# Optimization experiments

Hardware: AMD Instinct MI355X
Metric: run time of the kernel (lower is better)

## Reference

```python
import jax, jax.numpy as jnp
import numpy as np

N_NODES = 4096
N_EDGES = 131072
IN_DIM = 40
HID = 128
OUT = 128
GAT_H = 2
GAT_C = 64
D_MODEL = 128
N_HEAD = 4
FF_DIM = 2048
N_LAYERS = 2
EPS = 1e-5
NEG_SLOPE = 0.2


def _layer_norm(x, g, b):
    mu = x.mean(-1, keepdims=True)
    var = ((x - mu) ** 2).mean(-1, keepdims=True)
    return (x - mu) / jnp.sqrt(var + EPS) * g + b


def _gat_conv(h, src, dst, W, a_src, a_dst, bias):
    # PyG GATConv, concat=True, eval mode (no dropout). Self loops already in (src, dst).
    N = h.shape[0]
    xw = (h @ W.T).reshape(N, GAT_H, GAT_C)          # [N, H, C]
    al_src = (xw * a_src).sum(-1)                     # [N, H]
    al_dst = (xw * a_dst).sum(-1)                     # [N, H]
    e = jax.nn.leaky_relu(al_src[src] + al_dst[dst], NEG_SLOPE)  # [E, H]
    # segment softmax over incoming edges of each dst node
    m = jax.ops.segment_max(e, dst, num_segments=N)
    ex = jnp.exp(e - m[dst])
    s = jax.ops.segment_sum(ex, dst, num_segments=N)
    alpha = ex / (s[dst] + 1e-16)                     # [E, H]
    out = jax.ops.segment_sum(xw[src] * alpha[..., None], dst, num_segments=N)
    return out.reshape(N, GAT_H * GAT_C) + bias


def _encoder_layer(x, p):
    # post-norm nn.TransformerEncoderLayer, relu FFN, eval mode
    (in_w, in_b, out_w, out_b, ln1_g, ln1_b,
     ff_w1, ff_b1, ff_w2, ff_b2, ln2_g, ln2_b) = p
    S, E = x.shape
    Dh = E // N_HEAD
    qkv = x @ in_w.T + in_b                           # [S, 3E]
    q, k, v = [t.reshape(S, N_HEAD, Dh) for t in jnp.split(qkv, 3, axis=-1)]
    scores = jnp.einsum('shd,thd->hst', q, k) / jnp.asarray(np.sqrt(Dh), x.dtype)
    attn = jax.nn.softmax(scores, axis=-1)            # [H, S, S]
    o = jnp.einsum('hst,thd->shd', attn, v).reshape(S, E) @ out_w.T + out_b
    x = _layer_norm(x + o, ln1_g, ln1_b)
    ff = jax.nn.relu(x @ ff_w1.T + ff_b1) @ ff_w2.T + ff_b2
    return _layer_norm(x + ff, ln2_g, ln2_b)


def _forward(floats, edge_index):
    (x, enc_w1, enc_b1, enc_w2, enc_b2,
     gat_w, gat_asrc, gat_adst, gat_b,
     l0_in_w, l0_in_b, l0_out_w, l0_out_b, l0_ln1_g, l0_ln1_b,
     l0_ff_w1, l0_ff_b1, l0_ff_w2, l0_ff_b2, l0_ln2_g, l0_ln2_b,
     l1_in_w, l1_in_b, l1_out_w, l1_out_b, l1_ln1_g, l1_ln1_b,
     l1_ff_w1, l1_ff_b1, l1_ff_w2, l1_ff_b2, l1_ln2_g, l1_ln2_b) = floats
    N = x.shape[0]
    # encoder MLP
    h = jax.nn.relu(x @ enc_w1.T + enc_b1) @ enc_w2.T + enc_b2
    # add one self loop per node (GATConv add_self_loops semantics)
    loop = jnp.arange(N, dtype=edge_index.dtype)
    src = jnp.concatenate([edge_index[0], loop])
    dst = jnp.concatenate([edge_index[1], loop])
    h = _gat_conv(h, src, dst, gat_w, gat_asrc, gat_adst, gat_b)
    layers = [
        (l0_in_w, l0_in_b, l0_out_w, l0_out_b, l0_ln1_g, l0_ln1_b,
         l0_ff_w1, l0_ff_b1, l0_ff_w2, l0_ff_b2, l0_ln2_g, l0_ln2_b),
        (l1_in_w, l1_in_b, l1_out_w, l1_out_b, l1_ln1_g, l1_ln1_b,
         l1_ff_w1, l1_ff_b1, l1_ff_w2, l1_ff_b2, l1_ln2_g, l1_ln2_b),
    ]
    for p in layers:
        h = _encoder_layer(h, p)
    return h


def setup_inputs() -> dict:
    key = jax.random.key(0)
    ks = jax.random.split(key, 40)
    s = 0.05
    inp = {}
    inp['x'] = jax.random.normal(ks[0], (N_NODES, IN_DIM), dtype=jnp.float32)
    # edges with src != dst (self loops added inside reference)
    src = jax.random.randint(ks[1], (N_EDGES,), 0, N_NODES)
    off = jax.random.randint(ks[2], (N_EDGES,), 1, N_NODES)
    dst = (src + off) % N_NODES
    inp['edge_index'] = jnp.stack([src, dst]).astype(jnp.int64)
    inp['enc_w1'] = jax.random.normal(ks[3], (HID, IN_DIM)) * s
    inp['enc_b1'] = jnp.zeros((HID,), jnp.float32)
    inp['enc_w2'] = jax.random.normal(ks[4], (OUT, HID)) * s
    inp['enc_b2'] = jnp.zeros((OUT,), jnp.float32)
    inp['gat_w'] = jax.random.normal(ks[5], (GAT_H * GAT_C, OUT)) * s
    inp['gat_asrc'] = jax.random.normal(ks[6], (GAT_H, GAT_C)) * s
    inp['gat_adst'] = jax.random.normal(ks[7], (GAT_H, GAT_C)) * s
    inp['gat_b'] = jnp.zeros((GAT_H * GAT_C,), jnp.float32)
    for i in range(N_LAYERS):
        k = jax.random.split(ks[8 + i], 8)
        inp[f'l{i}_in_w'] = jax.random.normal(k[0], (3 * D_MODEL, D_MODEL)) * s
        inp[f'l{i}_in_b'] = jnp.zeros((3 * D_MODEL,), jnp.float32)
        inp[f'l{i}_out_w'] = jax.random.normal(k[1], (D_MODEL, D_MODEL)) * s
        inp[f'l{i}_out_b'] = jnp.zeros((D_MODEL,), jnp.float32)
        inp[f'l{i}_ln1_g'] = jnp.ones((D_MODEL,), jnp.float32)
        inp[f'l{i}_ln1_b'] = jnp.zeros((D_MODEL,), jnp.float32)
        inp[f'l{i}_ff_w1'] = jax.random.normal(k[2], (FF_DIM, D_MODEL)) * s
        inp[f'l{i}_ff_b1'] = jnp.zeros((FF_DIM,), jnp.float32)
        inp[f'l{i}_ff_w2'] = jax.random.normal(k[3], (D_MODEL, FF_DIM)) * s
        inp[f'l{i}_ff_b2'] = jnp.zeros((D_MODEL,), jnp.float32)
        inp[f'l{i}_ln2_g'] = jnp.ones((D_MODEL,), jnp.float32)
        inp[f'l{i}_ln2_b'] = jnp.zeros((D_MODEL,), jnp.float32)
    return inp


def reference(x, edge_index, enc_w1, enc_b1, enc_w2, enc_b2,
              gat_w, gat_asrc, gat_adst, gat_b,
              l0_in_w, l0_in_b, l0_out_w, l0_out_b, l0_ln1_g, l0_ln1_b,
              l0_ff_w1, l0_ff_b1, l0_ff_w2, l0_ff_b2, l0_ln2_g, l0_ln2_b,
              l1_in_w, l1_in_b, l1_out_w, l1_out_b, l1_ln1_g, l1_ln1_b,
              l1_ff_w1, l1_ff_b1, l1_ff_w2, l1_ff_b2, l1_ln2_g, l1_ln2_b):
    floats = (x, enc_w1, enc_b1, enc_w2, enc_b2,
              gat_w, gat_asrc, gat_adst, gat_b,
              l0_in_w, l0_in_b, l0_out_w, l0_out_b, l0_ln1_g, l0_ln1_b,
              l0_ff_w1, l0_ff_b1, l0_ff_w2, l0_ff_b2, l0_ln2_g, l0_ln2_b,
              l1_in_w, l1_in_b, l1_out_w, l1_out_b, l1_ln1_g, l1_ln1_b,
              l1_ff_w1, l1_ff_b1, l1_ff_w2, l1_ff_b2, l1_ln2_g, l1_ln2_b)
    return _forward(floats, edge_index)
```

## Files before the change

### kernel.cpp

```cpp
#include <hip/hip_runtime.h>
#include <hip/hip_bf16.h>

typedef __hip_bfloat16 bf16;

#define N_NODES 4096
#define IN_DIM  40
#define DM      128
#define FF_DIM  2048
#define GAT_H   2
#define GAT_C   64
#define NHEAD   4
#define DH      32
#define LN_EPS  1e-5f
#define KSPLIT  8
#define FSPLIT  4

typedef short s8v __attribute__((ext_vector_type(8)));
typedef float f4v __attribute__((ext_vector_type(4)));

__device__ __forceinline__ float anyload(const void* p, size_t i, int isbf) {
    if (isbf) return __bfloat162float(((const bf16*)p)[i]);
    return ((const float*)p)[i];
}
__device__ __forceinline__ int geti(const int* ei, int i, int is64) {
    return is64 ? ei[2 * (size_t)i] : ei[i];
}
__device__ __forceinline__ ushort tob(float v) {
    bf16 b = __float2bfloat16(v);
    return *(ushort*)&b;
}

__global__ void probe_kernel(const void* ones_vec, const int* ei, int* flags,
                             int* __restrict__ deg) {
    int i = blockIdx.x * 256 + threadIdx.x;
    if (i < N_NODES) deg[i] = 0;
    if (i == 0) {
        unsigned u = ((const unsigned*)ones_vec)[0];
        flags[0] = (u == 0x3F803F80u) ? 1 : 0;
        const unsigned* e = (const unsigned*)ei;
        flags[1] = (e[1] == 0u && e[3] == 0u && e[5] == 0u && e[7] == 0u) ? 1 : 0;
    }
}

__global__ __launch_bounds__(256) void enc1_mfma_kernel(const void* __restrict__ X,
                                                        const void* __restrict__ W,
                                                        const void* __restrict__ bias,
                                                        ushort* __restrict__ Cb,
                                                        const int* __restrict__ flags) {
    const int isbf = flags[0];
    const int t = threadIdx.x;
    const int w = t >> 6, lane = t & 63;
    const int col = lane & 15, quad = lane >> 4;
    const int wr = (w & 1) * 16, wc = (w >> 1) * 32;
    const int row0 = blockIdx.y * 32, col0 = blockIdx.x * 64;
    __shared__ __align__(16) ushort As[32 * 72];
    __shared__ __align__(16) ushort Ws[64 * 72];
    {
        int r = t >> 3, c0 = (t & 7) * 8;
#pragma unroll
        for (int j = 0; j < 8; ++j) {
            int c = c0 + j;
            float v = (c < IN_DIM) ? anyload(X, (size_t)(row0 + r) * IN_DIM + c, isbf) : 0.f;
            As[r * 72 + c] = tob(v);
        }
    }
#pragma unroll
    for (int i = 0; i < 2; ++i) {
        int idx = t + i * 256;
        int r = idx >> 3, c0 = (idx & 7) * 8;
#pragma unroll
        for (int j = 0; j < 8; ++j) {
            int c = c0 + j;
            float v = (c < IN_DIM) ? anyload(W, (size_t)(col0 + r) * IN_DIM + c, isbf) : 0.f;
            Ws[r * 72 + c] = tob(v);
        }
    }
    __syncthreads();
    f4v zero = {0.f, 0.f, 0.f, 0.f};
    f4v acc[2] = {zero, zero};
    s8v a0  = *(const s8v*)&As[(wr + col) * 72 + quad * 8];
    s8v a1  = *(const s8v*)&As[(wr + col) * 72 + 32 + quad * 8];
    s8v b00 = *(const s8v*)&Ws[(wc + col) * 72 + quad * 8];
    s8v b10 = *(const s8v*)&Ws[(wc + 16 + col) * 72 + quad * 8];
    s8v b01 = *(const s8v*)&Ws[(wc + col) * 72 + 32 + quad * 8];
    s8v b11 = *(const s8v*)&Ws[(wc + 16 + col) * 72 + 32 + quad * 8];
    acc[0] = __builtin_amdgcn_mfma_f32_16x16x32_bf16(a0, b00, acc[0], 0, 0, 0);
    acc[1] = __builtin_amdgcn_mfma_f32_16x16x32_bf16(a0, b10, acc[1], 0, 0, 0);
    acc[0] = __builtin_amdgcn_mfma_f32_16x16x32_bf16(a1, b01, acc[0], 0, 0, 0);
    acc[1] = __builtin_amdgcn_mfma_f32_16x16x32_bf16(a1, b11, acc[1], 0, 0, 0);
#pragma unroll
    for (int nc = 0; nc < 2; ++nc) {
        int cc = col0 + wc + nc * 16 + col;
        float bv = anyload(bias, cc, isbf);
#pragma unroll
        for (int r = 0; r < 4; ++r) {
            int rr = row0 + wr + quad * 4 + r;
            float v = fmaxf(acc[nc][r] + bv, 0.f);
            Cb[(size_t)rr * DM + cc] = tob(v);
        }
    }
}

#define K128STR 136
__global__ __launch_bounds__(256) void k128_gemm_kernel(const ushort* __restrict__ A,
                                                        const void* __restrict__ W,
                                                        const void* __restrict__ bias,
                                                        ushort* __restrict__ Cb,
                                                        ushort* __restrict__ vtb,
                                                        int N,
                                                        const int* __restrict__ flags,
                                                        int relu) {
    const int isbf = flags[0];
    const int t = threadIdx.x;
    const int w = t >> 6, lane = t & 63;
    const int col = lane & 15, quad = lane >> 4;
    const int wc = w * 16;
    const int row0 = blockIdx.y * 16, col0 = blockIdx.x * 64;
    __shared__ __align__(16) ushort As[16 * K128STR];
    __shared__ __align__(16) ushort Ws[64 * K128STR];
    {
        int ar = t >> 4, ac = (t & 15) * 8;
        *(uint4*)&As[ar * K128STR + ac] = *(const uint4*)&A[(size_t)(row0 + ar) * DM + ac];
    }
    if (isbf) {
        const ushort* Wb = (const ushort*)W;
#pragma unroll
        for (int i = 0; i < 4; ++i) {
            int idx = t + i * 256;
            int r = idx >> 4, c = (idx & 15) * 8;
            *(uint4*)&Ws[r * K128STR + c] = *(const uint4*)&Wb[(size_t)(col0 + r) * DM + c];
        }
    } else {
        const float* Wf = (const float*)W;
#pragma unroll
        for (int i = 0; i < 4; ++i) {
            int idx = t + i * 256;
            int r = idx >> 4, c = (idx & 15) * 8;
#pragma unroll
            for (int j = 0; j < 8; ++j)
                Ws[r * K128STR + c + j] = tob(Wf[(size_t)(col0 + r) * DM + c + j]);
        }
    }
    __syncthreads();
    f4v acc = {0.f, 0.f, 0.f, 0.f};
#pragma unroll
    for (int j = 0; j < 4; ++j) {
        s8v a = *(const s8v*)&As[col * K128STR + j * 32 + quad * 8];
        s8v b = *(const s8v*)&Ws[(wc + col) * K128STR + j * 32 + quad * 8];
        acc = __builtin_amdgcn_mfma_f32_16x16x32_bf16(a, b, acc, 0, 0, 0);
    }
    int cc = col0 + wc + col;
    float bv = bias ? anyload(bias, cc, isbf) : 0.f;
#pragma unroll
    for (int r = 0; r < 4; ++r) {
        int rr = row0 + quad * 4 + r;
        float v = acc[r] + bv;
        if (relu) v = fmaxf(v, 0.f);
        Cb[(size_t)rr * N + cc] = tob(v);
        if (vtb && cc >= 256) vtb[(size_t)(cc - 256) * N_NODES + rr] = tob(v);
    }
}

__global__ __launch_bounds__(256) void enc2_gat_kernel(const ushort* __restrict__ hid,
                                                       const void* __restrict__ w2,
                                                       const void* __restrict__ b2,
                                                       const void* __restrict__ gw,
                                                       const void* __restrict__ asrc,
                                                       const void* __restrict__ adst,
                                                       ushort* __restrict__ hb,
                                                       float* __restrict__ xw,
                                                       float* __restrict__ als,
                                                       float* __restrict__ ald,
                                                       const int* __restrict__ flags) {
    const int isbf = flags[0];
    const int t = threadIdx.x;
    const int w = t >> 6, lane = t & 63;
    const int col = lane & 15, quad = lane >> 4;
    const int row0 = blockIdx.x * 16;
    __shared__ __align__(16) ushort As[16 * K128STR];
    __shared__ __align__(16) ushort Ws[128 * K128STR];
    __shared__ float Cs[16][132];

    {
        int ar = t >> 4, ac = (t & 15) * 8;
        *(uint4*)&As[ar * K128STR + ac] = *(const uint4*)&hid[(size_t)(row0 + ar) * DM + ac];
    }
    if (isbf) {
        const ushort* Wb = (const ushort*)w2;
#pragma unroll
        for (int i = 0; i < 8; ++i) {
            int idx = t + i * 256;
            int r = idx >> 4, c = (idx & 15) * 8;
            *(uint4*)&Ws[r * K128STR + c] = *(const uint4*)&Wb[(size_t)r * DM + c];
        }
    } else {
        const float* Wf = (const float*)w2;
#pragma unroll
        for (int i = 0; i < 8; ++i) {
            int idx = t + i * 256;
            int r = idx >> 4, c = (idx & 15) * 8;
#pragma unroll
            for (int j = 0; j < 8; ++j)
                Ws[r * K128STR + c + j] = tob(Wf[(size_t)r * DM + c + j]);
        }
    }
    __syncthreads();
    f4v zero = {0.f, 0.f, 0.f, 0.f};
    f4v acc[2] = {zero, zero};
#pragma unroll
    for (int nc = 0; nc < 2; ++nc)
#pragma unroll
        for (int j = 0; j < 4; ++j) {
            s8v a = *(const s8v*)&As[col * K128STR + j * 32 + quad * 8];
            s8v b = *(const s8v*)&Ws[(w * 32 + nc * 16 + col) * K128STR + j * 32 + quad * 8];
            acc[nc] = __builtin_amdgcn_mfma_f32_16x16x32_bf16(a, b, acc[nc], 0, 0, 0);
        }
    __syncthreads();
#pragma unroll
    for (int nc = 0; nc < 2; ++nc) {
        int cc = w * 32 + nc * 16 + col;
        float bv = anyload(b2, cc, isbf);
#pragma unroll
        for (int r = 0; r < 4; ++r) {
            int row = quad * 4 + r;
            float v = acc[nc][r] + bv;
            ushort hv = tob(v);
            hb[(size_t)(row0 + row) * DM + cc] = hv;
            As[row * K128STR + cc] = hv;
        }
    }
    if (isbf) {
        const ushort* Wb = (const ushort*)gw;
#pragma unroll
        for (int i = 0; i < 8; ++i) {
            int idx = t + i * 256;
            int r = idx >> 4, c = (idx & 15) * 8;
            *(uint4*)&Ws[r * K128STR + c] = *(const uint4*)&Wb[(size_t)r * DM + c];
        }
    } else {
        const float* Wf = (const float*)gw;
#pragma unroll
        for (int i = 0; i < 8; ++i) {
            int idx = t + i * 256;
            int r = idx >> 4, c = (idx & 15) * 8;
#pragma unroll
            for (int j = 0; j < 8; ++j)
                Ws[r * K128STR + c + j] = tob(Wf[(size_t)r * DM + c + j]);
        }
    }
    __syncthreads();
    f4v acc2[2] = {zero, zero};
#pragma unroll
    for (int nc = 0; nc < 2; ++nc)
#pragma unroll
        for (int j = 0; j < 4; ++j) {
            s8v a = *(const s8v*)&As[col * K128STR + j * 32 + quad * 8];
            s8v b = *(const s8v*)&Ws[(w * 32 + nc * 16 + col) * K128STR + j * 32 + quad * 8];
            acc2[nc] = __builtin_amdgcn_mfma_f32_16x16x32_bf16(a, b, acc2[nc], 0, 0, 0);
        }
#pragma unroll
    for (int nc = 0; nc < 2; ++nc) {
        int cc = w * 32 + nc * 16 + col;
#pragma unroll
        for (int r = 0; r < 4; ++r) {
            int row = quad * 4 + r;
            float v = acc2[nc][r];
            xw[(size_t)(row0 + row) * DM + cc] = v;
            Cs[row][cc] = v;
        }
    }
    __syncthreads();
#pragma unroll
    for (int rr = 0; rr < 4; ++rr) {
        int row = w * 4 + rr;
        float x0 = Cs[row][lane], x1 = Cs[row][64 + lane];
        float s0 = x0 * anyload(asrc, lane, isbf);
        float d0 = x0 * anyload(adst, lane, isbf);
        float s1 = x1 * anyload(asrc, 64 + lane, isbf);
        float d1 = x1 * anyload(adst, 64 + lane, isbf);
#pragma unroll
        for (int o = 32; o >= 1; o >>= 1) {
            s0 += __shfl_xor(s0, o); d0 += __shfl_xor(d0, o);
            s1 += __shfl_xor(s1, o); d1 += __shfl_xor(d1, o);
        }
        if (lane == 0) {
            int n = row0 + row;
            als[n * 2 + 0] = s0; ald[n * 2 + 0] = d0;
            als[n * 2 + 1] = s1; ald[n * 2 + 1] = d1;
        }
    }
}

__global__ __launch_bounds__(256) void oproj_ln_kernel(const float* __restrict__ pO,
                                                       const float* __restrict__ pL,
                                                       const void* __restrict__ W,
                                                       const void* __restrict__ bias,
                                                       float* __restrict__ h,
                                                       ushort* __restrict__ hb,
                                                       const void* __restrict__ g,
                                                       const void* __restrict__ b,
                                                       const int* __restrict__ flags) {
    const int isbf = flags[0];
    const int t = threadIdx.x;
    const int w = t >> 6, lane = t & 63;
    const int col = lane & 15, quad = lane >> 4;
    const int row0 = blockIdx.x * 16;
    __shared__ __align__(16) ushort As[16 * K128STR];
    __shared__ __align__(16) ushort Ws[128 * K128STR];
    __shared__ float Cs[16][132];

    {
        int ar = t >> 4, ac = (t & 15) * 8;
        int rr = row0 + ar;
        int hh = ac >> 5, d0 = ac & 31;
        size_t qi0 = ((size_t)rr) * NHEAD + hh;
        float lsum = 0.f;
        float osum[8] = {};
#pragma unroll
        for (int kz = 0; kz < KSPLIT; ++kz) {
            size_t qi = qi0 + (size_t)kz * N_NODES * NHEAD;
            lsum += pL[qi];
            const float* po = &pO[qi * 32 + d0];
#pragma unroll
            for (int j = 0; j < 8; ++j) osum[j] += po[j];
        }
        float inv = 1.f / lsum;
#pragma unroll
        for (int j = 0; j < 8; ++j) As[ar * K128STR + ac + j] = tob(osum[j] * inv);
    }
    if (isbf) {
        const ushort* Wb = (const ushort*)W;
#pragma unroll
        for (int i = 0; i < 8; ++i) {
            int idx = t + i * 256;
            int r = idx >> 4, c = (idx & 15) * 8;
            *(uint4*)&Ws[r * K128STR + c] = *(const uint4*)&Wb[(size_t)r * DM + c];
        }
    } else {
        const float* Wf = (const float*)W;
#pragma unroll
        for (int i = 0; i < 8; ++i) {
            int idx = t + i * 256;
            int r = idx >> 4, c = (idx & 15) * 8;
#pragma unroll
            for (int j = 0; j < 8; ++j)
                Ws[r * K128STR + c + j] = tob(Wf[(size_t)r * DM + c + j]);
        }
    }
    __syncthreads();
    f4v zero = {0.f, 0.f, 0.f, 0.f};
    f4v acc[2] = {zero, zero};
#pragma unroll
    for (int nc = 0; nc < 2; ++nc)
#pragma unroll
        for (int j = 0; j < 4; ++j) {
            s8v a = *(const s8v*)&As[col * K128STR + j * 32 + quad * 8];
            s8v b = *(const s8v*)&Ws[(w * 32 + nc * 16 + col) * K128STR + j * 32 + quad * 8];
            acc[nc] = __builtin_amdgcn_mfma_f32_16x16x32_bf16(a, b, acc[nc], 0, 0, 0);
        }
#pragma unroll
    for (int nc = 0; nc < 2; ++nc) {
        int cc = w * 32 + nc * 16 + col;
        float bv = bias ? anyload(bias, cc, isbf) : 0.f;
#pragma unroll
        for (int r = 0; r < 4; ++r)
            Cs[quad * 4 + r][cc] = acc[nc][r] + bv;
    }
    __syncthreads();
#pragma unroll
    for (int rr = 0; rr < 4; ++rr) {
        int row = w * 4 + rr;
        size_t base = (size_t)(row0 + row) * DM;
        float v0 = h[base + lane] + Cs[row][lane];
        float v1 = h[base + 64 + lane] + Cs[row][64 + lane];
        float s = v0 + v1;
#pragma unroll
        for (int o = 32; o >= 1; o >>= 1) s += __shfl_xor(s, o);
        float mu = s * (1.f / DM);
        float d0 = v0 - mu, d1 = v1 - mu;
        float q = d0 * d0 + d1 * d1;
#pragma unroll
        for (int o = 32; o >= 1; o >>= 1) q += __shfl_xor(q, o);
        float rstd = rsqrtf(q * (1.f / DM) + LN_EPS);
        float o0 = d0 * rstd * anyload(g, lane, isbf) + anyload(b, lane, isbf);
        float o1 = d1 * rstd * anyload(g, 64 + lane, isbf) + anyload(b, 64 + lane, isbf);
        h[base + lane] = o0;       h[base + 64 + lane] = o1;
        hb[base + lane] = tob(o0); hb[base + 64 + lane] = tob(o1);
    }
}

__global__ __launch_bounds__(256) void mfma_gemm_splitk_kernel(const ushort* __restrict__ A,
                                                               const void* __restrict__ W,
                                                               float* __restrict__ Cpart,
                                                               int M, int N, int K, int kchunk,
                                                               const int* __restrict__ flags) {
    const int isbf = flags[0];
    const int t = threadIdx.x;
    const int w = t >> 6, lane = t & 63;
    const int col = lane & 15, quad = lane >> 4;
    const int wr = (w & 1) * 16, wc = (w >> 1) * 32;
    const int row0 = blockIdx.y * 32, col0 = blockIdx.x * 64;
    const int kz = blockIdx.z;
    const int k_beg = kz * kchunk, k_end = k_beg + kchunk;
    __shared__ __align__(16) ushort As[32 * 72];
    __shared__ __align__(16) ushort Ws[64 * 72];
    f4v zero = {0.f, 0.f, 0.f, 0.f};
    f4v acc[2] = {zero, zero};
    const int ar = t >> 3, ac = (t & 7) * 8;
    for (int k0 = k_beg; k0 < k_end; k0 += 64) {
        __syncthreads();
        *(uint4*)&As[ar * 72 + ac] = *(const uint4*)&A[(size_t)(row0 + ar) * K + k0 + ac];
        if (isbf) {
            const ushort* Wb = (const ushort*)W;
#pragma unroll
            for (int i = 0; i < 2; ++i) {
                int idx = t + i * 256;
                int r = idx >> 3, c = (idx & 7) * 8;
                *(uint4*)&Ws[r * 72 + c] = *(const uint4*)&Wb[(size_t)(col0 + r) * K + k0 + c];
            }
        } else {
            const float* Wf = (const float*)W;
#pragma unroll
            for (int i = 0; i < 2; ++i) {
                int idx = t + i * 256;
                int r = idx >> 3, c = (idx & 7) * 8;
#pragma unroll
                for (int j = 0; j < 8; ++j)
                    Ws[r * 72 + c + j] = tob(Wf[(size_t)(col0 + r) * K + k0 + c + j]);
            }
        }
        __syncthreads();
        s8v a0  = *(const s8v*)&As[(wr + col) * 72 + quad * 8];
        s8v a1  = *(const s8v*)&As[(wr + col) * 72 + 32 + quad * 8];
        s8v b00 = *(const s8v*)&Ws[(wc + col) * 72 + quad * 8];
        s8v b10 = *(const s8v*)&Ws[(wc + 16 + col) * 72 + quad * 8];
        s8v b01 = *(const s8v*)&Ws[(wc + col) * 72 + 32 + quad * 8];
        s8v b11 = *(const s8v*)&Ws[(wc + 16 + col) * 72 + 32 + quad * 8];
        acc[0] = __builtin_amdgcn_mfma_f32_16x16x32_bf16(a0, b00, acc[0], 0, 0, 0);
        acc[1] = __builtin_amdgcn_mfma_f32_16x16x32_bf16(a0, b10, acc[1], 0, 0, 0);
        acc[0] = __builtin_amdgcn_mfma_f32_16x16x32_bf16(a1, b01, acc[0], 0, 0, 0);
        acc[1] = __builtin_amdgcn_mfma_f32_16x16x32_bf16(a1, b11, acc[1], 0, 0, 0);
    }
#pragma unroll
    for (int nc = 0; nc < 2; ++nc) {
        int cc = col0 + wc + nc * 16 + col;
#pragma unroll
        for (int r = 0; r < 4; ++r) {
            int rr = row0 + wr + quad * 4 + r;
            Cpart[((size_t)kz * M + rr) * N + cc] = acc[nc][r];
        }
    }
}

__global__ void deg_hist_kernel(const int* __restrict__ ei, int E0,
                                int* __restrict__ deg, const int* __restrict__ flags) {
    const int is64 = flags[1];
    int e = blockIdx.x * 256 + threadIdx.x;
    int E = E0 + N_NODES;
    if (e >= E) return;
    int d = (e < E0) ? geti(ei, E0 + e, is64) : (e - E0);
    atomicAdd(&deg[d], 1);
}

__global__ __launch_bounds__(256) void scan_kernel(const int* __restrict__ deg,
                                                   int* __restrict__ rowptr,
                                                   int* __restrict__ cursor) {
    __shared__ int part[256];
    const int t = threadIdx.x;
    const int base = t * 16;
    int loc[16];
    int s = 0;
#pragma unroll
    for (int i = 0; i < 16; ++i) { loc[i] = s; s += deg[base + i]; }
    part[t] = s;
    __syncthreads();
    for (int d = 1; d < 256; d <<= 1) {
        int v = (t >= d) ? part[t - d] : 0;
        __syncthreads();
        part[t] += v;
        __syncthreads();
    }
    int prev = (t == 0) ? 0 : part[t - 1];
#pragma unroll
    for (int i = 0; i < 16; ++i) {
        int r = prev + loc[i];
        rowptr[base + i] = r;
        cursor[base + i] = r;
    }
    if (t == 255) rowptr[N_NODES] = part[255];
}

__global__ void scatter_kernel(const int* __restrict__ ei, int E0,
                               int* __restrict__ cursor, int* __restrict__ csr_src,
                               const int* __restrict__ flags) {
    const int is64 = flags[1];
    int e = blockIdx.x * 256 + threadIdx.x;
    int E = E0 + N_NODES;
    if (e >= E) return;
    int s = (e < E0) ? geti(ei, e, is64) : (e - E0);
    int d = (e < E0) ? geti(ei, E0 + e, is64) : (e - E0);
    int pos = atomicAdd(&cursor[d], 1);
    csr_src[pos] = s;
}

__global__ __launch_bounds__(256) void gat_gather_kernel(const int* __restrict__ rowptr,
                                                         const int* __restrict__ csr_src,
                                                         const float* __restrict__ als,
                                                         const float* __restrict__ ald,
                                                         const float* __restrict__ xw,
                                                         const void* __restrict__ gat_b,
                                                         float* __restrict__ hg,
                                                         ushort* __restrict__ hgb,
                                                         const int* __restrict__ flags) {
    const int isbf = flags[0];
    const int idx = blockIdx.x * 4 + (threadIdx.x >> 6);
    const int lane = threadIdx.x & 63;
    const int d = idx >> 1, hh = idx & 1;
    const int beg = rowptr[d], end = rowptr[d + 1];
    const float aldv = ald[d * 2 + hh];

    float mx = -3.0e38f;
    for (int i = beg + lane; i < end; i += 64) {
        int s = csr_src[i];
        float v = als[s * 2 + hh] + aldv;
        v = (v > 0.f) ? v : 0.2f * v;
        mx = fmaxf(mx, v);
    }
#pragma unroll
    for (int o = 32; o >= 1; o >>= 1) mx = fmaxf(mx, __shfl_xor(mx, o));
    float sm = 0.f;
    for (int i = beg + lane; i < end; i += 64) {
        int s = csr_src[i];
        float v = als[s * 2 + hh] + aldv;
        v = (v > 0.f) ? v : 0.2f * v;
        sm += __expf(v - mx);
    }
#pragma unroll
    for (int o = 32; o >= 1; o >>= 1) sm += __shfl_xor(sm, o);
    const float inv = 1.f / (sm + 1e-16f);

    float o_acc = 0.f;
    for (int i = beg; i < end; ++i) {
        int s = csr_src[i];
        float v = als[s * 2 + hh] + aldv;
        v = (v > 0.f) ? v : 0.2f * v;
        float alpha = __expf(v - mx) * inv;
        o_acc += alpha * xw[(size_t)s * DM + hh * GAT_C + lane];
    }
    float outv = o_acc + anyload(gat_b, hh * GAT_C + lane, isbf);
    size_t off = (size_t)d * DM + hh * GAT_C + lane;
    hg[off] = outv;
    hgb[off] = tob(outv);
}

#define KSTR 40
#define VSTR 136
#define PSTR 136
__global__ __launch_bounds__(256) void attn_mfma_kernel(const ushort* __restrict__ qkvb,
                                                        const ushort* __restrict__ vtb,
                                                        float* __restrict__ pO,
                                                        float* __restrict__ pL) {
    const int hh = blockIdx.y;
    const int kz = blockIdx.z;
    const int t = threadIdx.x;
    const int w = t >> 6;
    const int lane = t & 63;
    const int col = lane & 15;
    const int quad = lane >> 4;
    const int qr = blockIdx.x * 64 + w * 16;

    __shared__ __align__(16) ushort Ks[128 * KSTR];
    __shared__ __align__(16) ushort Vt[32 * VSTR];
    __shared__ __align__(16) ushort Pl[4][16 * PSTR];

    s8v aq = *(const s8v*)&qkvb[(size_t)(qr + col) * 384 + hh * 32 + quad * 8];

    f4v zero = {0.f, 0.f, 0.f, 0.f};
    f4v of[2] = {zero, zero};
    float lacc[4] = {0.f, 0.f, 0.f, 0.f};
    const float scale = 0.17677669529663687f;
    const int k_beg = kz * (N_NODES / KSPLIT);
    const int k_end = k_beg + (N_NODES / KSPLIT);

    for (int kt = k_beg; kt < k_end; kt += 128) {
        __syncthreads();
        for (int idx = t; idx < 512; idx += 256) {
            int r = idx >> 2, c = (idx & 3) * 8;
            *(uint4*)&Ks[r * KSTR + c] =
                *(const uint4*)&qkvb[(size_t)(kt + r) * 384 + 128 + hh * 32 + c];
        }
        for (int idx = t; idx < 512; idx += 256) {
            int d = idx >> 4, c = (idx & 15) * 8;
            *(uint4*)&Vt[d * VSTR + c] =
                *(const uint4*)&vtb[(size_t)(hh * 32 + d) * N_NODES + kt + c];
        }
        __syncthreads();

        f4v sf[8];
#pragma unroll
        for (int kb = 0; kb < 8; ++kb) {
            s8v bk = *(const s8v*)&Ks[(kb * 16 + col) * KSTR + quad * 8];
            sf[kb] = __builtin_amdgcn_mfma_f32_16x16x32_bf16(aq, bk, zero, 0, 0, 0);
        }
#pragma unroll
        for (int kb = 0; kb < 8; ++kb) {
#pragma unroll
            for (int r = 0; r < 4; ++r) {
                float p = __expf(sf[kb][r] * scale);
                lacc[r] += p;
                Pl[w][(quad * 4 + r) * PSTR + kb * 16 + col] = tob(p);
            }
        }
#pragma unroll
        for (int kc = 0; kc < 4; ++kc) {
            s8v ap = *(const s8v*)&Pl[w][col * PSTR + kc * 32 + quad * 8];
#pragma unroll
            for (int nc = 0; nc < 2; ++nc) {
                s8v bv = *(const s8v*)&Vt[(nc * 16 + col) * VSTR + kc * 32 + quad * 8];
                of[nc] = __builtin_amdgcn_mfma_f32_16x16x32_bf16(ap, bv, of[nc], 0, 0, 0);
            }
        }
    }
#pragma unroll
    for (int r = 0; r < 4; ++r) {
        float lv = lacc[r];
#pragma unroll
        for (int off = 1; off <= 8; off <<= 1) lv += __shfl_xor(lv, off);
        int row = quad * 4 + r;
        size_t qi = ((size_t)kz * N_NODES + qr + row) * NHEAD + hh;
#pragma unroll
        for (int nc = 0; nc < 2; ++nc)
            pO[qi * 32 + nc * 16 + col] = of[nc][r];
        if (col == 0) pL[qi] = lv;
    }
}

__global__ __launch_bounds__(256) void ln4_kernel(float* __restrict__ h,
                                                  const float* __restrict__ pC,
                                                  const void* __restrict__ fbias,
                                                  ushort* __restrict__ hb,
                                                  const void* __restrict__ g, const void* __restrict__ b,
                                                  void* __restrict__ outp,
                                                  const int* __restrict__ flags) {
    const int isbf = flags[0];
    const int row = blockIdx.x * 4 + (threadIdx.x >> 6);
    const int lane = threadIdx.x & 63;
    const size_t base = (size_t)row * DM;
    float y0 = anyload(fbias, lane, isbf), y1 = anyload(fbias, 64 + lane, isbf);
#pragma unroll
    for (int kz = 0; kz < FSPLIT; ++kz) {
        size_t pb = (size_t)kz * N_NODES * DM + base;
        y0 += pC[pb + lane];
        y1 += pC[pb + 64 + lane];
    }
    float v0 = h[base + lane] + y0;
    float v1 = h[base + 64 + lane] + y1;
    float s = v0 + v1;
#pragma unroll
    for (int o = 32; o >= 1; o >>= 1) s += __shfl_xor(s, o);
    float mu = s * (1.f / DM);
    float d0 = v0 - mu, d1 = v1 - mu;
    float q = d0 * d0 + d1 * d1;
#pragma unroll
    for (int o = 32; o >= 1; o >>= 1) q += __shfl_xor(q, o);
    float rstd = rsqrtf(q * (1.f / DM) + LN_EPS);
    float o0 = d0 * rstd * anyload(g, lane, isbf) + anyload(b, lane, isbf);
    float o1 = d1 * rstd * anyload(g, 64 + lane, isbf) + anyload(b, 64 + lane, isbf);
    h[base + lane] = o0;       h[base + 64 + lane] = o1;
    hb[base + lane] = tob(o0); hb[base + 64 + lane] = tob(o1);
    if (outp) {
        if (isbf) {
            ((ushort*)outp)[base + lane] = tob(o0);
            ((ushort*)outp)[base + 64 + lane] = tob(o1);
        } else {
            ((float*)outp)[base + lane] = o0;
            ((float*)outp)[base + 64 + lane] = o1;
        }
    }
}

extern "C" void kernel_launch(void* const* d_in, const int* in_sizes, int n_in,
                              void* d_out, int out_size, void* d_ws, size_t ws_size,
                              hipStream_t stream) {
    const void* x        = d_in[0];
    const int*  ei       = (const int*)d_in[1];
    const void* enc_w1   = d_in[2];
    const void* enc_b1   = d_in[3];
    const void* enc_w2   = d_in[4];
    const void* enc_b2   = d_in[5];
    const void* gat_w    = d_in[6];
    const void* gat_asrc = d_in[7];
    const void* gat_adst = d_in[8];
    const void* gat_b    = d_in[9];
    const void *in_w[2], *in_b[2], *out_w[2], *out_b[2], *ln1_g[2], *ln1_b[2];
    const void *ff_w1[2], *ff_b1[2], *ff_w2[2], *ff_b2[2], *ln2_g[2], *ln2_b[2];
    for (int L = 0; L < 2; ++L) {
        int base = 10 + L * 12;
        in_w[L]  = d_in[base + 0];
        in_b[L]  = d_in[base + 1];
        out_w[L] = d_in[base + 2];
        out_b[L] = d_in[base + 3];
        ln1_g[L] = d_in[base + 4];
        ln1_b[L] = d_in[base + 5];
        ff_w1[L] = d_in[base + 6];
        ff_b1[L] = d_in[base + 7];
        ff_w2[L] = d_in[base + 8];
        ff_b2[L] = d_in[base + 9];
        ln2_g[L] = d_in[base + 10];
        ln2_b[L] = d_in[base + 11];
    }
    const int E0 = in_sizes[1] / 2;
    const int E  = E0 + N_NODES;
    const size_t NN = N_NODES;

    int*    flags   = (int*)d_ws;
    float*  h       = (float*)d_ws + 64;
    ushort* hb      = (ushort*)(h + NN * DM);
    ushort* hid     = hb + NN * DM;
    ushort* qkvb    = hid + NN * DM;
    ushort* vtb     = qkvb + NN * 384;
    float*  pO      = (float*)(vtb + NN * DM);
    float*  pL      = pO + (size_t)KSPLIT * NN * NHEAD * 32;
    float*  pC      = pL + (size_t)KSPLIT * NN * NHEAD;
    ushort* ff1b    = (ushort*)(pC + (size_t)FSPLIT * NN * DM);
    float*  xw      = (float*)(ff1b + NN * FF_DIM);
    float*  als     = xw + NN * DM;
    float*  ald     = als + NN * GAT_H;
    int*    deg     = (int*)(ald + NN * GAT_H);
    int*    rowptr  = deg + N_NODES;
    int*    cursor  = rowptr + N_NODES + 1;
    int*    csr_src = cursor + N_NODES;

    dim3 blk(256);

    probe_kernel<<<dim3(16), blk, 0, stream>>>(ln1_g[0], ei, flags, deg);
    deg_hist_kernel<<<dim3((E + 255) / 256), blk, 0, stream>>>(ei, E0, deg, flags);
    scan_kernel<<<dim3(1), blk, 0, stream>>>(deg, rowptr, cursor);
    scatter_kernel<<<dim3((E + 255) / 256), blk, 0, stream>>>(ei, E0, cursor, csr_src, flags);

    enc1_mfma_kernel<<<dim3(DM / 64, N_NODES / 32), blk, 0, stream>>>(
        x, enc_w1, enc_b1, hid, flags);
    enc2_gat_kernel<<<dim3(N_NODES / 16), blk, 0, stream>>>(
        hid, enc_w2, enc_b2, gat_w, gat_asrc, gat_adst, hb, xw, als, ald, flags);
    gat_gather_kernel<<<dim3(N_NODES * GAT_H / 4), blk, 0, stream>>>(
        rowptr, csr_src, als, ald, xw, gat_b, h, hb, flags);

    for (int L = 0; L < 2; ++L) {
        k128_gemm_kernel<<<dim3(3 * DM / 64, N_NODES / 16), blk, 0, stream>>>(
            hb, in_w[L], in_b[L], qkvb, vtb, 3 * DM, flags, 0);
        attn_mfma_kernel<<<dim3(N_NODES / 64, NHEAD, KSPLIT), blk, 0, stream>>>(
            qkvb, vtb, pO, pL);
        oproj_ln_kernel<<<dim3(N_NODES / 16), blk, 0, stream>>>(
            pO, pL, out_w[L], out_b[L], h, hb, ln1_g[L], ln1_b[L], flags);
        k128_gemm_kernel<<<dim3(FF_DIM / 64, N_NODES / 16), blk, 0, stream>>>(
            hb, ff_w1[L], ff_b1[L], ff1b, nullptr, FF_DIM, flags, 1);
        mfma_gemm_splitk_kernel<<<dim3(DM / 64, N_NODES / 32, FSPLIT), blk, 0, stream>>>(
            ff1b, ff_w2[L], pC, N_NODES, DM, FF_DIM, FF_DIM / FSPLIT, flags);
        ln4_kernel<<<dim3(N_NODES / 4), blk, 0, stream>>>(
            h, pC, ff_b2[L], hb, ln2_g[L], ln2_b[L],
            (L == 1) ? d_out : nullptr, flags);
    }
}
```

Baseline: 337.5 us.

## Pre-convert weights to bf16, fuse encoder+GAT, fuse FF2 with LayerNorm, retile GEMMs

Adds a single up-front kernel that converts all weight matrices into one bf16 buffer, so the GEMM kernels no longer branch on dtype or convert per tile. The two encoder GEMMs and the GAT projection are merged into one kernel that keeps intermediates in shared memory. The split-K FF2 GEMM and its reduction/LayerNorm kernel are replaced by one fused ff2ln kernel, which removes the partial-sum buffer. The QKV/FF1 GEMMs move to 32-row tiles, and attention split-K drops from 8 to 4. The cost is an extra conversion pass over roughly 1.2M weights on every call, and the fused FF2 kernel has less parallelism.

```diff
diff --git a/kernel.cpp b/kernel.cpp
--- a/kernel.cpp
+++ b/kernel.cpp
@@ -12,11 +12,20 @@
 #define NHEAD   4
 #define DH      32
 #define LN_EPS  1e-5f
-#define KSPLIT  8
-#define FSPLIT  4
+#define KSPLIT  4
 
 typedef short s8v __attribute__((ext_vector_type(8)));
 typedef float f4v __attribute__((ext_vector_type(4)));
+
+#define WO_ENC1 0
+#define WO_ENC2 8192
+#define WO_GAT  24576
+#define WO_L(L) (40960 + (L) * 589824)
+#define WO_IN(L)  (WO_L(L))
+#define WO_OUT(L) (WO_L(L) + 49152)
+#define WO_FF1(L) (WO_L(L) + 65536)
+#define WO_FF2(L) (WO_L(L) + 327680)
+#define WBUF_ELEMS 1220608
 
 __device__ __forceinline__ float anyload(const void* p, size_t i, int isbf) {
     if (isbf) return __bfloat162float(((const bf16*)p)[i]);
@@ -42,136 +51,53 @@
     }
 }
 
-__global__ __launch_bounds__(256) void enc1_mfma_kernel(const void* __restrict__ X,
-                                                        const void* __restrict__ W,
-                                                        const void* __restrict__ bias,
-                                                        ushort* __restrict__ Cb,
-                                                        const int* __restrict__ flags) {
+__global__ __launch_bounds__(256) void wconv_kernel(const void* enc_w1, const void* enc_w2,
+                                                    const void* gat_w,
+                                                    const void* in_w0, const void* out_w0,
+                                                    const void* ff_w10, const void* ff_w20,
+                                                    const void* in_w1, const void* out_w1,
+                                                    const void* ff_w11, const void* ff_w21,
+                                                    ushort* __restrict__ wbuf,
+                                                    const int* __restrict__ flags) {
     const int isbf = flags[0];
-    const int t = threadIdx.x;
-    const int w = t >> 6, lane = t & 63;
-    const int col = lane & 15, quad = lane >> 4;
-    const int wr = (w & 1) * 16, wc = (w >> 1) * 32;
-    const int row0 = blockIdx.y * 32, col0 = blockIdx.x * 64;
-    __shared__ __align__(16) ushort As[32 * 72];
-    __shared__ __align__(16) ushort Ws[64 * 72];
-    {
-        int r = t >> 3, c0 = (t & 7) * 8;
-#pragma unroll
-        for (int j = 0; j < 8; ++j) {
-            int c = c0 + j;
-            float v = (c < IN_DIM) ? anyload(X, (size_t)(row0 + r) * IN_DIM + c, isbf) : 0.f;
-            As[r * 72 + c] = tob(v);
-        }
-    }
-#pragma unroll
-    for (int i = 0; i < 2; ++i) {
-        int idx = t + i * 256;
-        int r = idx >> 3, c0 = (idx & 7) * 8;
-#pragma unroll
-        for (int j = 0; j < 8; ++j) {
-            int c = c0 + j;
-            float v = (c < IN_DIM) ? anyload(W, (size_t)(col0 + r) * IN_DIM + c, isbf) : 0.f;
-            Ws[r * 72 + c] = tob(v);
-        }
-    }
-    __syncthreads();
-    f4v zero = {0.f, 0.f, 0.f, 0.f};
-    f4v acc[2] = {zero, zero};
-    s8v a0  = *(const s8v*)&As[(wr + col) * 72 + quad * 8];
-    s8v a1  = *(const s8v*)&As[(wr + col) * 72 + 32 + quad * 8];
-    s8v b00 = *(const s8v*)&Ws[(wc + col) * 72 + quad * 8];
-    s8v b10 = *(const s8v*)&Ws[(wc + 16 + col) * 72 + quad * 8];
-    s8v b01 = *(const s8v*)&Ws[(wc + col) * 72 + 32 + quad * 8];
-    s8v b11 = *(const s8v*)&Ws[(wc + 16 + col) * 72 + 32 + quad * 8];
-    acc[0] = __builtin_amdgcn_mfma_f32_16x16x32_bf16(a0, b00, acc[0], 0, 0, 0);
-    acc[1] = __builtin_amdgcn_mfma_f32_16x16x32_bf16(a0, b10, acc[1], 0, 0, 0);
-    acc[0] = __builtin_amdgcn_mfma_f32_16x16x32_bf16(a1, b01, acc[0], 0, 0, 0);
-    acc[1] = __builtin_amdgcn_mfma_f32_16x16x32_bf16(a1, b11, acc[1], 0, 0, 0);
-#pragma unroll
-    for (int nc = 0; nc < 2; ++nc) {
-        int cc = col0 + wc + nc * 16 + col;
-        float bv = anyload(bias, cc, isbf);
-#pragma unroll
-        for (int r = 0; r < 4; ++r) {
-            int rr = row0 + wr + quad * 4 + r;
-            float v = fmaxf(acc[nc][r] + bv, 0.f);
-            Cb[(size_t)rr * DM + cc] = tob(v);
-        }
+    int base = (blockIdx.x * 256 + threadIdx.x) * 4;
+#pragma unroll
+    for (int j = 0; j < 4; ++j) {
+        int i = base + j;
+        if (i < WO_ENC2) {
+            int r = i >> 6, c = i & 63;
+            float v = (c < IN_DIM) ? anyload(enc_w1, (size_t)r * IN_DIM + c, isbf) : 0.f;
+            wbuf[i] = tob(v);
+            continue;
+        }
+        const void* s;
+        int si;
+        if      (i < WO_GAT)     { s = enc_w2; si = i - WO_ENC2; }
+        else if (i < WO_L(0))    { s = gat_w;  si = i - WO_GAT; }
+        else if (i < WO_OUT(0))  { s = in_w0;  si = i - WO_IN(0); }
+        else if (i < WO_FF1(0))  { s = out_w0; si = i - WO_OUT(0); }
+        else if (i < WO_FF2(0))  { s = ff_w10; si = i - WO_FF1(0); }
+        else if (i < WO_L(1))    { s = ff_w20; si = i - WO_FF2(0); }
+        else if (i < WO_OUT(1))  { s = in_w1;  si = i - WO_IN(1); }
+        else if (i < WO_FF1(1))  { s = out_w1; si = i - WO_OUT(1); }
+        else if (i < WO_FF2(1))  { s = ff_w11; si = i - WO_FF1(1); }
+        else                     { s = ff_w21; si = i - WO_FF2(1); }
+        wbuf[i] = isbf ? ((const ushort*)s)[si] : tob(((const float*)s)[si]);
     }
 }
 
 #define K128STR 136
-__global__ __launch_bounds__(256) void k128_gemm_kernel(const ushort* __restrict__ A,
-                                                        const void* __restrict__ W,
-                                                        const void* __restrict__ bias,
-                                                        ushort* __restrict__ Cb,
-                                                        ushort* __restrict__ vtb,
-                                                        int N,
-                                                        const int* __restrict__ flags,
-                                                        int relu) {
-    const int isbf = flags[0];
-    const int t = threadIdx.x;
-    const int w = t >> 6, lane = t & 63;
-    const int col = lane & 15, quad = lane >> 4;
-    const int wc = w * 16;
-    const int row0 = blockIdx.y * 16, col0 = blockIdx.x * 64;
-    __shared__ __align__(16) ushort As[16 * K128STR];
-    __shared__ __align__(16) ushort Ws[64 * K128STR];
-    {
-        int ar = t >> 4, ac = (t & 15) * 8;
-        *(uint4*)&As[ar * K128STR + ac] = *(const uint4*)&A[(size_t)(row0 + ar) * DM + ac];
-    }
-    if (isbf) {
-        const ushort* Wb = (const ushort*)W;
-#pragma unroll
-        for (int i = 0; i < 4; ++i) {
-            int idx = t + i * 256;
-            int r = idx >> 4, c = (idx & 15) * 8;
-            *(uint4*)&Ws[r * K128STR + c] = *(const uint4*)&Wb[(size_t)(col0 + r) * DM + c];
-        }
-    } else {
-        const float* Wf = (const float*)W;
-#pragma unroll
-        for (int i = 0; i < 4; ++i) {
-            int idx = t + i * 256;
-            int r = idx >> 4, c = (idx & 15) * 8;
-#pragma unroll
-            for (int j = 0; j < 8; ++j)
-                Ws[r * K128STR + c + j] = tob(Wf[(size_t)(col0 + r) * DM + c + j]);
-        }
-    }
-    __syncthreads();
-    f4v acc = {0.f, 0.f, 0.f, 0.f};
-#pragma unroll
-    for (int j = 0; j < 4; ++j) {
-        s8v a = *(const s8v*)&As[col * K128STR + j * 32 + quad * 8];
-        s8v b = *(const s8v*)&Ws[(wc + col) * K128STR + j * 32 + quad * 8];
-        acc = __builtin_amdgcn_mfma_f32_16x16x32_bf16(a, b, acc, 0, 0, 0);
-    }
-    int cc = col0 + wc + col;
-    float bv = bias ? anyload(bias, cc, isbf) : 0.f;
-#pragma unroll
-    for (int r = 0; r < 4; ++r) {
-        int rr = row0 + quad * 4 + r;
-        float v = acc[r] + bv;
-        if (relu) v = fmaxf(v, 0.f);
-        Cb[(size_t)rr * N + cc] = tob(v);
-        if (vtb && cc >= 256) vtb[(size_t)(cc - 256) * N_NODES + rr] = tob(v);
-    }
-}
-
-__global__ __launch_bounds__(256) void enc2_gat_kernel(const ushort* __restrict__ hid,
-                                                       const void* __restrict__ w2,
-                                                       const void* __restrict__ b2,
-                                                       const void* __restrict__ gw,
-                                                       const void* __restrict__ asrc,
-                                                       const void* __restrict__ adst,
-                                                       ushort* __restrict__ hb,
-                                                       float* __restrict__ xw,
-                                                       float* __restrict__ als,
-                                                       float* __restrict__ ald,
-                                                       const int* __restrict__ flags) {
+
+__global__ __launch_bounds__(256) void encgat_kernel(const void* __restrict__ X,
+                                                     const void* __restrict__ b1v,
+                                                     const void* __restrict__ b2v,
+                                                     const ushort* __restrict__ wbuf,
+                                                     const void* __restrict__ asrc,
+                                                     const void* __restrict__ adst,
+                                                     float* __restrict__ xwout,
+                                                     float* __restrict__ als,
+                                                     float* __restrict__ ald,
+                                                     const int* __restrict__ flags) {
     const int isbf = flags[0];
     const int t = threadIdx.x;
     const int w = t >> 6, lane = t & 63;
@@ -182,90 +108,94 @@
     __shared__ float Cs[16][132];
 
     {
-        int ar = t >> 4, ac = (t & 15) * 8;
-        *(uint4*)&As[ar * K128STR + ac] = *(const uint4*)&hid[(size_t)(row0 + ar) * DM + ac];
-    }
-    if (isbf) {
-        const ushort* Wb = (const ushort*)w2;
-#pragma unroll
-        for (int i = 0; i < 8; ++i) {
-            int idx = t + i * 256;
-            int r = idx >> 4, c = (idx & 15) * 8;
-            *(uint4*)&Ws[r * K128STR + c] = *(const uint4*)&Wb[(size_t)r * DM + c];
-        }
-    } else {
-        const float* Wf = (const float*)w2;
-#pragma unroll
-        for (int i = 0; i < 8; ++i) {
-            int idx = t + i * 256;
-            int r = idx >> 4, c = (idx & 15) * 8;
-#pragma unroll
-            for (int j = 0; j < 8; ++j)
-                Ws[r * K128STR + c + j] = tob(Wf[(size_t)r * DM + c + j]);
-        }
+        int r = t >> 4, c0 = (t & 15) * 4;
+#pragma unroll
+        for (int j = 0; j < 4; ++j) {
+            int c = c0 + j;
+            float v = (c < IN_DIM) ? anyload(X, (size_t)(row0 + r) * IN_DIM + c, isbf) : 0.f;
+            As[r * K128STR + c] = tob(v);
+        }
+    }
+#pragma unroll
+    for (int i = 0; i < 4; ++i) {
+        int idx = t + i * 256;
+        int r = idx >> 3, c = (idx & 7) * 8;
+        *(uint4*)&Ws[r * 72 + c] = *(const uint4*)&wbuf[WO_ENC1 + r * 64 + c];
     }
     __syncthreads();
     f4v zero = {0.f, 0.f, 0.f, 0.f};
-    f4v acc[2] = {zero, zero};
-#pragma unroll
-    for (int nc = 0; nc < 2; ++nc)
-#pragma unroll
-        for (int j = 0; j < 4; ++j) {
-            s8v a = *(const s8v*)&As[col * K128STR + j * 32 + quad * 8];
-            s8v b = *(const s8v*)&Ws[(w * 32 + nc * 16 + col) * K128STR + j * 32 + quad * 8];
-            acc[nc] = __builtin_amdgcn_mfma_f32_16x16x32_bf16(a, b, acc[nc], 0, 0, 0);
-        }
+    f4v acc1[2] = {zero, zero};
+    {
+        s8v a0 = *(const s8v*)&As[col * K128STR + quad * 8];
+        s8v a1 = *(const s8v*)&As[col * K128STR + 32 + quad * 8];
+#pragma unroll
+        for (int nc = 0; nc < 2; ++nc) {
+            s8v b0 = *(const s8v*)&Ws[(w * 32 + nc * 16 + col) * 72 + quad * 8];
+            s8v b1 = *(const s8v*)&Ws[(w * 32 + nc * 16 + col) * 72 + 32 + quad * 8];
+            acc1[nc] = __builtin_amdgcn_mfma_f32_16x16x32_bf16(a0, b0, acc1[nc], 0, 0, 0);
+            acc1[nc] = __builtin_amdgcn_mfma_f32_16x16x32_bf16(a1, b1, acc1[nc], 0, 0, 0);
+        }
+    }
     __syncthreads();
 #pragma unroll
     for (int nc = 0; nc < 2; ++nc) {
         int cc = w * 32 + nc * 16 + col;
-        float bv = anyload(b2, cc, isbf);
+        float bv = anyload(b1v, cc, isbf);
+#pragma unroll
+        for (int r = 0; r < 4; ++r)
+            As[(quad * 4 + r) * K128STR + cc] = tob(fmaxf(acc1[nc][r] + bv, 0.f));
+    }
+#pragma unroll
+    for (int i = 0; i < 8; ++i) {
+        int idx = t + i * 256;
+        int r = idx >> 4, c = (idx & 15) * 8;
+        *(uint4*)&Ws[r * K128STR + c] = *(const uint4*)&wbuf[WO_ENC2 + r * DM + c];
+    }
+    __syncthreads();
+    f4v acc2[2] = {zero, zero};
+#pragma unroll
+    for (int j = 0; j < 4; ++j) {
+        s8v a = *(const s8v*)&As[col * K128STR + j * 32 + quad * 8];
+#pragma unroll
+        for (int nc = 0; nc < 2; ++nc) {
+            s8v b = *(const s8v*)&Ws[(w * 32 + nc * 16 + col) * K128STR + j * 32 + quad * 8];
+            acc2[nc] = __builtin_amdgcn_mfma_f32_16x16x32_bf16(a, b, acc2[nc], 0, 0, 0);
+        }
+    }
+    __syncthreads();
+#pragma unroll
+    for (int nc = 0; nc < 2; ++nc) {
+        int cc = w * 32 + nc * 16 + col;
+        float bv = anyload(b2v, cc, isbf);
+#pragma unroll
+        for (int r = 0; r < 4; ++r)
+            As[(quad * 4 + r) * K128STR + cc] = tob(acc2[nc][r] + bv);
+    }
+#pragma unroll
+    for (int i = 0; i < 8; ++i) {
+        int idx = t + i * 256;
+        int r = idx >> 4, c = (idx & 15) * 8;
+        *(uint4*)&Ws[r * K128STR + c] = *(const uint4*)&wbuf[WO_GAT + r * DM + c];
+    }
+    __syncthreads();
+    f4v acc3[2] = {zero, zero};
+#pragma unroll
+    for (int j = 0; j < 4; ++j) {
+        s8v a = *(const s8v*)&As[col * K128STR + j * 32 + quad * 8];
+#pragma unroll
+        for (int nc = 0; nc < 2; ++nc) {
+            s8v b = *(const s8v*)&Ws[(w * 32 + nc * 16 + col) * K128STR + j * 32 + quad * 8];
+            acc3[nc] = __builtin_amdgcn_mfma_f32_16x16x32_bf16(a, b, acc3[nc], 0, 0, 0);
+        }
+    }
+#pragma unroll
+    for (int nc = 0; nc < 2; ++nc) {
+        int cc = w * 32 + nc * 16 + col;
 #pragma unroll
         for (int r = 0; r < 4; ++r) {
             int row = quad * 4 + r;
-            float v = acc[nc][r] + bv;
-            ushort hv = tob(v);
-            hb[(size_t)(row0 + row) * DM + cc] = hv;
-            As[row * K128STR + cc] = hv;
-        }
-    }
-    if (isbf) {
-        const ushort* Wb = (const ushort*)gw;
-#pragma unroll
-        for (int i = 0; i < 8; ++i) {
-            int idx = t + i * 256;
-            int r = idx >> 4, c = (idx & 15) * 8;
-            *(uint4*)&Ws[r * K128STR + c] = *(const uint4*)&Wb[(size_t)r * DM + c];
-        }
-    } else {
-        const float* Wf = (const float*)gw;
-#pragma unroll
-        for (int i = 0; i < 8; ++i) {
-            int idx = t + i * 256;
-            int r = idx >> 4, c = (idx & 15) * 8;
-#pragma unroll
-            for (int j = 0; j < 8; ++j)
-                Ws[r * K128STR + c + j] = tob(Wf[(size_t)r * DM + c + j]);
-        }
-    }
-    __syncthreads();
-    f4v acc2[2] = {zero, zero};
-#pragma unroll
-    for (int nc = 0; nc < 2; ++nc)
-#pragma unroll
-        for (int j = 0; j < 4; ++j) {
-            s8v a = *(const s8v*)&As[col * K128STR + j * 32 + quad * 8];
-            s8v b = *(const s8v*)&Ws[(w * 32 + nc * 16 + col) * K128STR + j * 32 + quad * 8];
-            acc2[nc] = __builtin_amdgcn_mfma_f32_16x16x32_bf16(a, b, acc2[nc], 0, 0, 0);
-        }
-#pragma unroll
-    for (int nc = 0; nc < 2; ++nc) {
-        int cc = w * 32 + nc * 16 + col;
-#pragma unroll
-        for (int r = 0; r < 4; ++r) {
-            int row = quad * 4 + r;
-            float v = acc2[nc][r];
-            xw[(size_t)(row0 + row) * DM + cc] = v;
+            float v = acc3[nc][r];
+            xwout[(size_t)(row0 + row) * DM + cc] = v;
             Cs[row][cc] = v;
         }
     }
@@ -291,9 +221,64 @@
     }
 }
 
+__global__ __launch_bounds__(256) void gemm32_kernel(const ushort* __restrict__ A,
+                                                     const ushort* __restrict__ Wb,
+                                                     const void* __restrict__ bias,
+                                                     ushort* __restrict__ Cb,
+                                                     ushort* __restrict__ vtb,
+                                                     int N,
+                                                     const int* __restrict__ flags,
+                                                     int relu) {
+    const int isbf = flags[0];
+    const int t = threadIdx.x;
+    const int w = t >> 6, lane = t & 63;
+    const int col = lane & 15, quad = lane >> 4;
+    const int wr = (w & 1) * 16, wc = (w >> 1) * 32;
+    const int row0 = blockIdx.y * 32, col0 = blockIdx.x * 64;
+    __shared__ __align__(16) ushort As[32 * K128STR];
+    __shared__ __align__(16) ushort Ws[64 * K128STR];
+#pragma unroll
+    for (int i = 0; i < 2; ++i) {
+        int idx = t + i * 256;
+        int r = idx >> 4, c = (idx & 15) * 8;
+        *(uint4*)&As[r * K128STR + c] = *(const uint4*)&A[(size_t)(row0 + r) * DM + c];
+    }
+#pragma unroll
+    for (int i = 0; i < 4; ++i) {
+        int idx = t + i * 256;
+        int r = idx >> 4, c = (idx & 15) * 8;
+        *(uint4*)&Ws[r * K128STR + c] = *(const uint4*)&Wb[(size_t)(col0 + r) * DM + c];
+    }
+    __syncthreads();
+    f4v zero = {0.f, 0.f, 0.f, 0.f};
+    f4v acc[2] = {zero, zero};
+#pragma unroll
+    for (int j = 0; j < 4; ++j) {
+        s8v a = *(const s8v*)&As[(wr + col) * K128STR + j * 32 + quad * 8];
+#pragma unroll
+        for (int nc = 0; nc < 2; ++nc) {
+            s8v b = *(const s8v*)&Ws[(wc + nc * 16 + col) * K128STR + j * 32 + quad * 8];
+            acc[nc] = __builtin_amdgcn_mfma_f32_16x16x32_bf16(a, b, acc[nc], 0, 0, 0);
+        }
+    }
+#pragma unroll
+    for (int nc = 0; nc < 2; ++nc) {
+        int cc = col0 + wc + nc * 16 + col;
+        float bv = bias ? anyload(bias, cc, isbf) : 0.f;
+#pragma unroll
+        for (int r = 0; r < 4; ++r) {
+            int rr = row0 + wr + quad * 4 + r;
+            float v = acc[nc][r] + bv;
+            if (relu) v = fmaxf(v, 0.f);
+            Cb[(size_t)rr * N + cc] = tob(v);
+            if (vtb && cc >= 256) vtb[(size_t)(cc - 256) * N_NODES + rr] = tob(v);
+        }
+    }
+}
+
 __global__ __launch_bounds__(256) void oproj_ln_kernel(const float* __restrict__ pO,
                                                        const float* __restrict__ pL,
-                                                       const void* __restrict__ W,
+                                                       const ushort* __restrict__ Wb,
                                                        const void* __restrict__ bias,
                                                        float* __restrict__ h,
                                                        ushort* __restrict__ hb,
@@ -328,36 +313,24 @@
 #pragma unroll
         for (int j = 0; j < 8; ++j) As[ar * K128STR + ac + j] = tob(osum[j] * inv);
     }
-    if (isbf) {
-        const ushort* Wb = (const ushort*)W;
-#pragma unroll
-        for (int i = 0; i < 8; ++i) {
-            int idx = t + i * 256;
-            int r = idx >> 4, c = (idx & 15) * 8;
-            *(uint4*)&Ws[r * K128STR + c] = *(const uint4*)&Wb[(size_t)r * DM + c];
-        }
-    } else {
-        const float* Wf = (const float*)W;
-#pragma unroll
-        for (int i = 0; i < 8; ++i) {
-            int idx = t + i * 256;
-            int r = idx >> 4, c = (idx & 15) * 8;
-#pragma unroll
-            for (int j = 0; j < 8; ++j)
-                Ws[r * K128STR + c + j] = tob(Wf[(size_t)r * DM + c + j]);
-        }
+#pragma unroll
+    for (int i = 0; i < 8; ++i) {
+        int idx = t + i * 256;
+        int r = idx >> 4, c = (idx & 15) * 8;
+        *(uint4*)&Ws[r * K128STR + c] = *(const uint4*)&Wb[(size_t)r * DM + c];
     }
     __syncthreads();
     f4v zero = {0.f, 0.f, 0.f, 0.f};
     f4v acc[2] = {zero, zero};
 #pragma unroll
-    for (int nc = 0; nc < 2; ++nc)
-#pragma unroll
-        for (int j = 0; j < 4; ++j) {
-            s8v a = *(const s8v*)&As[col * K128STR + j * 32 + quad * 8];
+    for (int j = 0; j < 4; ++j) {
+        s8v a = *(const s8v*)&As[col * K128STR + j * 32 + quad * 8];
+#pragma unroll
+        for (int nc = 0; nc < 2; ++nc) {
             s8v b = *(const s8v*)&Ws[(w * 32 + nc * 16 + col) * K128STR + j * 32 + quad * 8];
             acc[nc] = __builtin_amdgcn_mfma_f32_16x16x32_bf16(a, b, acc[nc], 0, 0, 0);
         }
+    }
 #pragma unroll
     for (int nc = 0; nc < 2; ++nc) {
         int cc = w * 32 + nc * 16 + col;
@@ -389,65 +362,81 @@
     }
 }
 
-__global__ __launch_bounds__(256) void mfma_gemm_splitk_kernel(const ushort* __restrict__ A,
-                                                               const void* __restrict__ W,
-                                                               float* __restrict__ Cpart,
-                                                               int M, int N, int K, int kchunk,
-                                                               const int* __restrict__ flags) {
+__global__ __launch_bounds__(512) void ff2ln_kernel(const ushort* __restrict__ A,
+                                                    const ushort* __restrict__ Wb,
+                                                    const void* __restrict__ fbias,
+                                                    float* __restrict__ h,
+                                                    ushort* __restrict__ hb,
+                                                    const void* __restrict__ g,
+                                                    const void* __restrict__ b,
+                                                    void* __restrict__ outp,
+                                                    const int* __restrict__ flags) {
     const int isbf = flags[0];
     const int t = threadIdx.x;
     const int w = t >> 6, lane = t & 63;
     const int col = lane & 15, quad = lane >> 4;
-    const int wr = (w & 1) * 16, wc = (w >> 1) * 32;
-    const int row0 = blockIdx.y * 32, col0 = blockIdx.x * 64;
-    const int kz = blockIdx.z;
-    const int k_beg = kz * kchunk, k_end = k_beg + kchunk;
-    __shared__ __align__(16) ushort As[32 * 72];
-    __shared__ __align__(16) ushort Ws[64 * 72];
+    const int row0 = blockIdx.x * 16;
+    __shared__ __align__(16) ushort As[16 * K128STR];
+    __shared__ __align__(16) ushort Ws[128 * K128STR];
+    __shared__ float Cs[16][132];
     f4v zero = {0.f, 0.f, 0.f, 0.f};
-    f4v acc[2] = {zero, zero};
-    const int ar = t >> 3, ac = (t & 7) * 8;
-    for (int k0 = k_beg; k0 < k_end; k0 += 64) {
+    f4v acc = zero;
+    for (int k0 = 0; k0 < FF_DIM; k0 += 128) {
         __syncthreads();
-        *(uint4*)&As[ar * 72 + ac] = *(const uint4*)&A[(size_t)(row0 + ar) * K + k0 + ac];
-        if (isbf) {
-            const ushort* Wb = (const ushort*)W;
-#pragma unroll
-            for (int i = 0; i < 2; ++i) {
-                int idx = t + i * 256;
-                int r = idx >> 3, c = (idx & 7) * 8;
-                *(uint4*)&Ws[r * 72 + c] = *(const uint4*)&Wb[(size_t)(col0 + r) * K + k0 + c];
+        if (t < 256) {
+            int ar = t >> 4, ac = (t & 15) * 8;
+            *(uint4*)&As[ar * K128STR + ac] =
+                *(const uint4*)&A[(size_t)(row0 + ar) * FF_DIM + k0 + ac];
+        }
+#pragma unroll
+        for (int i = 0; i < 4; ++i) {
+            int idx = t + i * 512;
+            int r = idx >> 4, c = (idx & 15) * 8;
+            *(uint4*)&Ws[r * K128STR + c] = *(const uint4*)&Wb[(size_t)r * FF_DIM + k0 + c];
+        }
+        __syncthreads();
+#pragma unroll
+        for (int j = 0; j < 4; ++j) {
+            s8v a = *(const s8v*)&As[col * K128STR + j * 32 + quad * 8];
+            s8v bb = *(const s8v*)&Ws[(w * 16 + col) * K128STR + j * 32 + quad * 8];
+            acc = __builtin_amdgcn_mfma_f32_16x16x32_bf16(a, bb, acc, 0, 0, 0);
+        }
+    }
+    {
+        int cc = w * 16 + col;
+        float bv = anyload(fbias, cc, isbf);
+#pragma unroll
+        for (int r = 0; r < 4; ++r)
+            Cs[quad * 4 + r][cc] = acc[r] + bv;
+    }
+    __syncthreads();
+#pragma unroll
+    for (int rr = 0; rr < 2; ++rr) {
+        int row = w * 2 + rr;
+        size_t base = (size_t)(row0 + row) * DM;
+        float v0 = h[base + lane] + Cs[row][lane];
+        float v1 = h[base + 64 + lane] + Cs[row][64 + lane];
+        float s = v0 + v1;
+#pragma unroll
+        for (int o = 32; o >= 1; o >>= 1) s += __shfl_xor(s, o);
+        float mu = s * (1.f / DM);
+        float d0 = v0 - mu, d1 = v1 - mu;
+        float q = d0 * d0 + d1 * d1;
+#pragma unroll
+        for (int o = 32; o >= 1; o >>= 1) q += __shfl_xor(q, o);
+        float rstd = rsqrtf(q * (1.f / DM) + LN_EPS);
+        float o0 = d0 * rstd * anyload(g, lane, isbf) + anyload(b, lane, isbf);
+        float o1 = d1 * rstd * anyload(g, 64 + lane, isbf) + anyload(b, 64 + lane, isbf);
+        h[base + lane] = o0;       h[base + 64 + lane] = o1;
+        hb[base + lane] = tob(o0); hb[base + 64 + lane] = tob(o1);
+        if (outp) {
+            if (isbf) {
+                ((ushort*)outp)[base + lane] = tob(o0);
+                ((ushort*)outp)[base + 64 + lane] = tob(o1);
+            } else {
+                ((float*)outp)[base + lane] = o0;
+                ((float*)outp)[base + 64 + lane] = o1;
             }
-        } else {
-            const float* Wf = (const float*)W;
-#pragma unroll
-            for (int i = 0; i < 2; ++i) {
-                int idx = t + i * 256;
-                int r = idx >> 3, c = (idx & 7) * 8;
-#pragma unroll
-                for (int j = 0; j < 8; ++j)
-                    Ws[r * 72 + c + j] = tob(Wf[(size_t)(col0 + r) * K + k0 + c + j]);
-            }
-        }
-        __syncthreads();
-        s8v a0  = *(const s8v*)&As[(wr + col) * 72 + quad * 8];
-        s8v a1  = *(const s8v*)&As[(wr + col) * 72 + 32 + quad * 8];
-        s8v b00 = *(const s8v*)&Ws[(wc + col) * 72 + quad * 8];
-        s8v b10 = *(const s8v*)&Ws[(wc + 16 + col) * 72 + quad * 8];
-        s8v b01 = *(const s8v*)&Ws[(wc + col) * 72 + 32 + quad * 8];
-        s8v b11 = *(const s8v*)&Ws[(wc + 16 + col) * 72 + 32 + quad * 8];
-        acc[0] = __builtin_amdgcn_mfma_f32_16x16x32_bf16(a0, b00, acc[0], 0, 0, 0);
-        acc[1] = __builtin_amdgcn_mfma_f32_16x16x32_bf16(a0, b10, acc[1], 0, 0, 0);
-        acc[0] = __builtin_amdgcn_mfma_f32_16x16x32_bf16(a1, b01, acc[0], 0, 0, 0);
-        acc[1] = __builtin_amdgcn_mfma_f32_16x16x32_bf16(a1, b11, acc[1], 0, 0, 0);
-    }
-#pragma unroll
-    for (int nc = 0; nc < 2; ++nc) {
-        int cc = col0 + wc + nc * 16 + col;
-#pragma unroll
-        for (int r = 0; r < 4; ++r) {
-            int rr = row0 + wr + quad * 4 + r;
-            Cpart[((size_t)kz * M + rr) * N + cc] = acc[nc][r];
         }
     }
 }
@@ -632,50 +621,6 @@
         for (int nc = 0; nc < 2; ++nc)
             pO[qi * 32 + nc * 16 + col] = of[nc][r];
         if (col == 0) pL[qi] = lv;
-    }
-}
-
-__global__ __launch_bounds__(256) void ln4_kernel(float* __restrict__ h,
-                                                  const float* __restrict__ pC,
-                                                  const void* __restrict__ fbias,
-                                                  ushort* __restrict__ hb,
-                                                  const void* __restrict__ g, const void* __restrict__ b,
-                                                  void* __restrict__ outp,
-                                                  const int* __restrict__ flags) {
-    const int isbf = flags[0];
-    const int row = blockIdx.x * 4 + (threadIdx.x >> 6);
-    const int lane = threadIdx.x & 63;
-    const size_t base = (size_t)row * DM;
-    float y0 = anyload(fbias, lane, isbf), y1 = anyload(fbias, 64 + lane, isbf);
-#pragma unroll
-    for (int kz = 0; kz < FSPLIT; ++kz) {
-        size_t pb = (size_t)kz * N_NODES * DM + base;
-        y0 += pC[pb + lane];
-        y1 += pC[pb + 64 + lane];
-    }
-    float v0 = h[base + lane] + y0;
-    float v1 = h[base + 64 + lane] + y1;
-    float s = v0 + v1;
-#pragma unroll
-    for (int o = 32; o >= 1; o >>= 1) s += __shfl_xor(s, o);
-    float mu = s * (1.f / DM);
-    float d0 = v0 - mu, d1 = v1 - mu;
-    float q = d0 * d0 + d1 * d1;
-#pragma unroll
-    for (int o = 32; o >= 1; o >>= 1) q += __shfl_xor(q, o);
-    float rstd = rsqrtf(q * (1.f / DM) + LN_EPS);
-    float o0 = d0 * rstd * anyload(g, lane, isbf) + anyload(b, lane, isbf);
-    float o1 = d1 * rstd * anyload(g, 64 + lane, isbf) + anyload(b, 64 + lane, isbf);
-    h[base + lane] = o0;       h[base + 64 + lane] = o1;
-    hb[base + lane] = tob(o0); hb[base + 64 + lane] = tob(o1);
-    if (outp) {
-        if (isbf) {
-            ((ushort*)outp)[base + lane] = tob(o0);
-            ((ushort*)outp)[base + 64 + lane] = tob(o1);
-        } else {
-            ((float*)outp)[base + lane] = o0;
-            ((float*)outp)[base + 64 + lane] = o1;
-        }
     }
 }
 
@@ -716,14 +661,13 @@
     int*    flags   = (int*)d_ws;
     float*  h       = (float*)d_ws + 64;
     ushort* hb      = (ushort*)(h + NN * DM);
-    ushort* hid     = hb + NN * DM;
-    ushort* qkvb    = hid + NN * DM;
+    ushort* qkvb    = hb + NN * DM;
     ushort* vtb     = qkvb + NN * 384;
-    float*  pO      = (float*)(vtb + NN * DM);
+    ushort* ff1b    = vtb + NN * DM;
+    ushort* wbuf    = ff1b + NN * FF_DIM;
+    float*  pO      = (float*)(wbuf + WBUF_ELEMS);
     float*  pL      = pO + (size_t)KSPLIT * NN * NHEAD * 32;
-    float*  pC      = pL + (size_t)KSPLIT * NN * NHEAD;
-    ushort* ff1b    = (ushort*)(pC + (size_t)FSPLIT * NN * DM);
-    float*  xw      = (float*)(ff1b + NN * FF_DIM);
+    float*  xw      = pL + (size_t)KSPLIT * NN * NHEAD;
     float*  als     = xw + NN * DM;
     float*  ald     = als + NN * GAT_H;
     int*    deg     = (int*)(ald + NN * GAT_H);
@@ -734,30 +678,29 @@
     dim3 blk(256);
 
     probe_kernel<<<dim3(16), blk, 0, stream>>>(ln1_g[0], ei, flags, deg);
+    wconv_kernel<<<dim3(WBUF_ELEMS / 1024), blk, 0, stream>>>(
+        enc_w1, enc_w2, gat_w, in_w[0], out_w[0], ff_w1[0], ff_w2[0],
+        in_w[1], out_w[1], ff_w1[1], ff_w2[1], wbuf, flags);
     deg_hist_kernel<<<dim3((E + 255) / 256), blk, 0, stream>>>(ei, E0, deg, flags);
     scan_kernel<<<dim3(1), blk, 0, stream>>>(deg, rowptr, cursor);
     scatter_kernel<<<dim3((E + 255) / 256), blk, 0, stream>>>(ei, E0, cursor, csr_src, flags);
 
-    enc1_mfma_kernel<<<dim3(DM / 64, N_NODES / 32), blk, 0, stream>>>(
-        x, enc_w1, enc_b1, hid, flags);
-    enc2_gat_kernel<<<dim3(N_NODES / 16), blk, 0, stream>>>(
-        hid, enc_w2, enc_b2, gat_w, gat_asrc, gat_adst, hb, xw, als, ald, flags);
+    encgat_kernel<<<dim3(N_NODES / 16), blk, 0, stream>>>(
+        x, enc_b1, enc_b2, wbuf, gat_asrc, gat_adst, xw, als, ald, flags);
     gat_gather_kernel<<<dim3(N_NODES * GAT_H / 4), blk, 0, stream>>>(
         rowptr, csr_src, als, ald, xw, gat_b, h, hb, flags);
 
     for (int L = 0; L < 2; ++L) {
-        k128_gemm_kernel<<<dim3(3 * DM / 64, N_NODES / 16), blk, 0, stream>>>(
-            hb, in_w[L], in_b[L], qkvb, vtb, 3 * DM, flags, 0);
+        gemm32_kernel<<<dim3(3 * DM / 64, N_NODES / 32), blk, 0, stream>>>(
+            hb, wbuf + WO_IN(L), in_b[L], qkvb, vtb, 3 * DM, flags, 0);
         attn_mfma_kernel<<<dim3(N_NODES / 64, NHEAD, KSPLIT), blk, 0, stream>>>(
             qkvb, vtb, pO, pL);
         oproj_ln_kernel<<<dim3(N_NODES / 16), blk, 0, stream>>>(
-            pO, pL, out_w[L], out_b[L], h, hb, ln1_g[L], ln1_b[L], flags);
-        k128_gemm_kernel<<<dim3(FF_DIM / 64, N_NODES / 16), blk, 0, stream>>>(
-            hb, ff_w1[L], ff_b1[L], ff1b, nullptr, FF_DIM, flags, 1);
-        mfma_gemm_splitk_kernel<<<dim3(DM / 64, N_NODES / 32, FSPLIT), blk, 0, stream>>>(
-            ff1b, ff_w2[L], pC, N_NODES, DM, FF_DIM, FF_DIM / FSPLIT, flags);
-        ln4_kernel<<<dim3(N_NODES / 4), blk, 0, stream>>>(
-            h, pC, ff_b2[L], hb, ln2_g[L], ln2_b[L],
+            pO, pL, wbuf + WO_OUT(L), out_b[L], h, hb, ln1_g[L], ln1_b[L], flags);
+        gemm32_kernel<<<dim3(FF_DIM / 64, N_NODES / 32), blk, 0, stream>>>(
+            hb, wbuf + WO_FF1(L), ff_b1[L], ff1b, nullptr, FF_DIM, flags, 1);
+        ff2ln_kernel<<<dim3(N_NODES / 16), dim3(512), 0, stream>>>(
+            ff1b, wbuf + WO_FF2(L), ff_b2[L], h, hb, ln2_g[L], ln2_b[L],
             (L == 1) ? d_out : nullptr, flags);
     }
 }
```

Measured after the change: 330.4 us. 2.1% less time.
